# Performance work log

Hardware: AMD Instinct MI355X
Metric: run time of the kernel (lower is better)

The kernel has to match this reference:

```python
import jax, jax.numpy as jnp
import numpy as np

CAPACITY_GAMMA = 0.5

def setup_inputs() -> dict:
    key = jax.random.key(0)
    k1, k2 = jax.random.split(key)
    B, S, H = 4, 4096, 2048
    hidden_states = jax.random.normal(k1, (B, S, H), dtype=jnp.float32)
    gate_w = jax.random.normal(k2, (1, H), dtype=jnp.float32) * (1.0 / np.sqrt(H))
    return {"hidden_states": hidden_states, "gate_w": gate_w}

def reference(hidden_states, gate_w):
    # scores: [B, S] = Linear(H -> 1, no bias) then squeeze
    scores = jnp.einsum("bsh,h->bs", hidden_states, gate_w[0])
    B, S = scores.shape
    k = int(CAPACITY_GAMMA * S)
    if k >= S:
        mask = jnp.ones_like(scores)
    else:
        _, top_idx = jax.lax.top_k(scores, k)          # [B, k]
        batch_idx = jnp.arange(B)[:, None]              # [B, 1]
        mask = jnp.zeros_like(scores).at[batch_idx, top_idx].set(1.0)
    return (mask, scores)
```

## Files before the change

### kernel.cpp

```cpp
#include <hip/hip_runtime.h>

#define BB 4
#define SS 4096
#define HH 2048
#define KK 2048

typedef float f4 __attribute__((ext_vector_type(4)));


__global__ void __launch_bounds__(256, 4)
scores_kernel(const float* __restrict__ hs,
              const float* __restrict__ gw,
              float* __restrict__ scores) {
    __shared__ f4 gls[512];
    int t = threadIdx.x;
    const f4* g4 = reinterpret_cast<const f4*>(gw);
    gls[t]       = g4[t];
    gls[t + 256] = g4[t + 256];
    __syncthreads();

    int wave = t >> 6, lane = t & 63;
    int g = lane >> 4, p = lane & 15;
    int row = blockIdx.x * 16 + wave * 4 + g;
    const f4* r4 = reinterpret_cast<const f4*>(hs + (size_t)row * HH);

    f4 A[8], B[8];
#pragma unroll
    for (int i = 0; i < 8; ++i)
        A[i] = __builtin_nontemporal_load(&r4[i * 16 + p]);

    double acc0 = 0.0, acc1 = 0.0;
#pragma unroll
    for (int c = 0; c < 4; ++c) {
        if (c < 3) {
#pragma unroll
            for (int i = 0; i < 8; ++i)
                B[i] = __builtin_nontemporal_load(&r4[(c + 1) * 128 + i * 16 + p]);
        }
#pragma unroll
        for (int i = 0; i < 8; ++i) {
            f4 gg = gls[c * 128 + i * 16 + p];
            f4 aa = A[i];
            acc0 = fma((double)aa.x, (double)gg.x, acc0);
            acc1 = fma((double)aa.y, (double)gg.y, acc1);
            acc0 = fma((double)aa.z, (double)gg.z, acc0);
            acc1 = fma((double)aa.w, (double)gg.w, acc1);
        }
        if (c < 3) {
#pragma unroll
            for (int i = 0; i < 8; ++i) A[i] = B[i];
        }
    }

    double s = acc0 + acc1;
    s += __shfl_xor(s, 8);
    s += __shfl_xor(s, 4);
    s += __shfl_xor(s, 2);
    s += __shfl_xor(s, 1);
    if (p == 0) scores[row] = (float)s;
}


__device__ __forceinline__ unsigned to_ord(float f) {
    unsigned u = __float_as_uint(f);
    return (u & 0x80000000u) ? ~u : (u | 0x80000000u);
}

__device__ __forceinline__ int dpp_wave_sum(int v) {
    v += __builtin_amdgcn_update_dpp(0, v, 0x111, 0xF, 0xF, true);
    v += __builtin_amdgcn_update_dpp(0, v, 0x112, 0xF, 0xF, true);
    v += __builtin_amdgcn_update_dpp(0, v, 0x114, 0xF, 0xF, true);
    v += __builtin_amdgcn_update_dpp(0, v, 0x118, 0xF, 0xF, true);
    v += __builtin_amdgcn_update_dpp(0, v, 0x142, 0xF, 0xF, true);
    v += __builtin_amdgcn_update_dpp(0, v, 0x143, 0xF, 0xF, true);
    return __builtin_amdgcn_readlane(v, 63);
}

__global__ void __launch_bounds__(256)
topk_mask_kernel(const float* __restrict__ scores, float* __restrict__ mask) {
    int b = blockIdx.x, t = threadIdx.x;
    int w = t >> 6, lane = t & 63;
    const f4* sc4 = reinterpret_cast<const f4*>(scores + b * SS);

    f4 v[4];
#pragma unroll
    for (int i = 0; i < 4; ++i) v[i] = sc4[t * 4 + i];

    unsigned ord[16];
#pragma unroll
    for (int i = 0; i < 4; ++i) {
        ord[4 * i + 0] = to_ord(v[i].x);
        ord[4 * i + 1] = to_ord(v[i].y);
        ord[4 * i + 2] = to_ord(v[i].z);
        ord[4 * i + 3] = to_ord(v[i].w);
    }

    __shared__ int wsum[2][4];
    __shared__ int tts[256];

    unsigned cur = 0u, thresh = 0u;
    bool exact = false;
    int par = 0;
    for (int bit = 31; bit >= 0; --bit) {
        unsigned cand = cur | (1u << bit);
        int c = 0;
#pragma unroll
        for (int i = 0; i < 16; ++i) c += (ord[i] >= cand) ? 1 : 0;
        int ws = dpp_wave_sum(c);
        if (lane == 0) wsum[par][w] = ws;
        __syncthreads();
        int total = wsum[par][0] + wsum[par][1] + wsum[par][2] + wsum[par][3];
        par ^= 1;
        if (total >= KK) cur = cand;
        if (total == KK) { exact = true; thresh = cand; break; }
    }

    f4* m4 = reinterpret_cast<f4*>(mask + b * SS);

    if (exact) {
#pragma unroll
        for (int i = 0; i < 4; ++i) {
            f4 m;
            m.x = (ord[4 * i + 0] >= thresh) ? 1.0f : 0.0f;
            m.y = (ord[4 * i + 1] >= thresh) ? 1.0f : 0.0f;
            m.z = (ord[4 * i + 2] >= thresh) ? 1.0f : 0.0f;
            m.w = (ord[4 * i + 3] >= thresh) ? 1.0f : 0.0f;
            m4[t * 4 + i] = m;
        }
        return;
    }

    int cgl = 0, ttl = 0;
#pragma unroll
    for (int i = 0; i < 16; ++i) {
        cgl += (ord[i] > cur) ? 1 : 0;
        ttl += (ord[i] == cur) ? 1 : 0;
    }
    int cgw = dpp_wave_sum(cgl);
    if (lane == 0) wsum[0][w] = cgw;
    tts[t] = ttl;
    __syncthreads();
    int cg = wsum[0][0] + wsum[0][1] + wsum[0][2] + wsum[0][3];
    int r = KK - cg;
    if (t == 0) {
        int acc = 0;
        for (int i = 0; i < 256; ++i) { int x = tts[i]; tts[i] = acc; acc += x; }
    }
    __syncthreads();
    int pfx = tts[t];
#pragma unroll
    for (int i = 0; i < 4; ++i) {
        float mm[4];
#pragma unroll
        for (int j = 0; j < 4; ++j) {
            unsigned o = ord[4 * i + j];
            bool gt  = o > cur;
            bool tie = o == cur;
            mm[j] = (gt || (tie && pfx < r)) ? 1.0f : 0.0f;
            if (tie) ++pfx;
        }
        f4 m; m.x = mm[0]; m.y = mm[1]; m.z = mm[2]; m.w = mm[3];
        m4[t * 4 + i] = m;
    }
}

extern "C" void kernel_launch(void* const* d_in, const int* in_sizes, int n_in,
                              void* d_out, int out_size, void* d_ws, size_t ws_size,
                              hipStream_t stream) {
    const float* hs = (const float*)d_in[0];
    const float* gw = (const float*)d_in[1];
    float* out    = (float*)d_out;
    float* mask   = out;
    float* scores = out + BB * SS;

    scores_kernel<<<BB * SS / 16, 256, 0, stream>>>(hs, gw, scores);
    topk_mask_kernel<<<BB, 256, 0, stream>>>(scores, mask);
}
```

Measured before the change: 32.48 us.

## Assign whole rows to waves in scores kernel and raise occupancy

Each wave now handles two full rows in sequence, with all 64 lanes covering one row through 8 float4 loads each, replacing the scheme where 16-lane groups walked a quarter-row in four prefetched chunks. The grid doubles to 2048 blocks of 8 rows, and launch bounds ask for 8 blocks per CU, cutting register use by dropping the B prefetch buffer. The aim is more memory-level parallelism from higher occupancy and fully coalesced row loads. The cost is a full 64-lane shuffle reduction per row and no overlap of loads with the FP64 math inside a wave.

```diff
diff --git a/kernel.cpp b/kernel.cpp
--- a/kernel.cpp
+++ b/kernel.cpp
@@ -7,8 +7,7 @@
 
 typedef float f4 __attribute__((ext_vector_type(4)));
 
-
-__global__ void __launch_bounds__(256, 4)
+__global__ void __launch_bounds__(256, 8)
 scores_kernel(const float* __restrict__ hs,
               const float* __restrict__ gw,
               float* __restrict__ scores) {
@@ -20,44 +19,33 @@
     __syncthreads();
 
     int wave = t >> 6, lane = t & 63;
-    int g = lane >> 4, p = lane & 15;
-    int row = blockIdx.x * 16 + wave * 4 + g;
-    const f4* r4 = reinterpret_cast<const f4*>(hs + (size_t)row * HH);
+    int row0 = blockIdx.x * 8 + wave * 2;
 
-    f4 A[8], B[8];
+#pragma unroll 1
+    for (int rr = 0; rr < 2; ++rr) {
+        int row = row0 + rr;
+        const f4* r4 = reinterpret_cast<const f4*>(hs + (size_t)row * HH);
+        f4 A[8];
 #pragma unroll
-    for (int i = 0; i < 8; ++i)
-        A[i] = __builtin_nontemporal_load(&r4[i * 16 + p]);
+        for (int i = 0; i < 8; ++i)
+            A[i] = __builtin_nontemporal_load(&r4[i * 64 + lane]);
 
-    double acc0 = 0.0, acc1 = 0.0;
-#pragma unroll
-    for (int c = 0; c < 4; ++c) {
-        if (c < 3) {
-#pragma unroll
-            for (int i = 0; i < 8; ++i)
-                B[i] = __builtin_nontemporal_load(&r4[(c + 1) * 128 + i * 16 + p]);
-        }
+        double acc0 = 0.0, acc1 = 0.0;
 #pragma unroll
         for (int i = 0; i < 8; ++i) {
-            f4 gg = gls[c * 128 + i * 16 + p];
+            f4 gg = gls[i * 64 + lane];
             f4 aa = A[i];
             acc0 = fma((double)aa.x, (double)gg.x, acc0);
             acc1 = fma((double)aa.y, (double)gg.y, acc1);
             acc0 = fma((double)aa.z, (double)gg.z, acc0);
             acc1 = fma((double)aa.w, (double)gg.w, acc1);
         }
-        if (c < 3) {
+        double s = acc0 + acc1;
 #pragma unroll
-            for (int i = 0; i < 8; ++i) A[i] = B[i];
-        }
+        for (int off = 32; off >= 1; off >>= 1)
+            s += __shfl_down(s, off);
+        if (lane == 0) scores[row] = (float)s;
     }
-
-    double s = acc0 + acc1;
-    s += __shfl_xor(s, 8);
-    s += __shfl_xor(s, 4);
-    s += __shfl_xor(s, 2);
-    s += __shfl_xor(s, 1);
-    if (p == 0) scores[row] = (float)s;
 }
 
 
@@ -173,6 +161,6 @@
     float* mask   = out;
     float* scores = out + BB * SS;
 
-    scores_kernel<<<BB * SS / 16, 256, 0, stream>>>(hs, gw, scores);
+    scores_kernel<<<BB * SS / 8, 256, 0, stream>>>(hs, gw, scores);
     topk_mask_kernel<<<BB, 256, 0, stream>>>(scores, mask);
 }
```

Result: slower. 81.17 us (+149.9%).
